# Optimization experiments

Hardware: AMD Instinct MI355X
Metric: run time of the kernel (lower is better)

The kernel has to match this reference:

```python
import jax, jax.numpy as jnp
import numpy as np

IN_C, OUT_C, K = 256, 256, 3

def setup_inputs() -> dict:
    key = jax.random.key(0)
    kx, kw, kb = jax.random.split(key, 3)
    x = jax.random.normal(kx, (32, IN_C, 56, 56), dtype=jnp.float32)
    # kaiming-like scale for conv weight
    fan_in = IN_C * K * K
    weight = jax.random.normal(kw, (OUT_C, IN_C, K, K), dtype=jnp.float32) / np.sqrt(fan_in)
    bias = jax.random.normal(kb, (OUT_C,), dtype=jnp.float32) * 0.01
    return {"x": x, "weight": weight, "bias": bias}

def reference(x, weight, bias):
    # SparseConv2d computes an (approximately lossless, threshold=1e-6)
    # block-sparse conv2d; exact math == dense conv2d, stride 1, pad 1.
    y = jax.lax.conv_general_dilated(
        x, weight,
        window_strides=(1, 1),
        padding=((1, 1), (1, 1)),
        dimension_numbers=("NCHW", "OIHW", "NCHW"),
    )
    return y + bias[None, :, None, None]
```

## Files before the change

### kernel.cpp

```cpp
#include <hip/hip_runtime.h>
#include <hip/hip_bf16.h>

#define IN_C  256
#define OUT_C 256
#define HH 56
#define WW 56
#define NN 32
#define XT_H 58
#define XT_W 64
#define WT_BYTES (8*9*256*32*2)

#define XS_BYTES 24576
#define WS_TAP   8192
#define LDS_TOTAL (2*XS_BYTES + 4*WS_TAP)

using short8 = __attribute__((ext_vector_type(8))) short;
using f32x4  = __attribute__((ext_vector_type(4))) float;

__device__ __forceinline__ void gload_lds16(const void* g, void* l) {
  __builtin_amdgcn_global_load_lds((const __attribute__((address_space(1))) void*)g,
                                   (__attribute__((address_space(3))) void*)l,
                                   16, 0, 0);
}

#define VMWAIT(N) asm volatile("s_waitcnt vmcnt(" #N ")" ::: "memory")

__global__ void k_wconv(const float* __restrict__ w, __hip_bfloat16* __restrict__ wt) {
  int idx = blockIdx.x * 256 + threadIdx.x;
  if (idx >= OUT_C * IN_C * 9) return;
  int kw = idx % 3; int t1 = idx / 3;
  int kh = t1 % 3;  int t2 = t1 / 3;
  int ic = t2 % IN_C; int oc = t2 / IN_C;
  int tap = kh * 3 + kw;
  int chunk = ic >> 5, ic5 = ic & 31;
  wt[(((chunk * 9 + tap) * 256 + oc) * 32) + ic5] = __float2bfloat16(w[idx]);
}

__global__ void k_xpad(__hip_bfloat16* __restrict__ xt) {
  int cell = blockIdx.x * 256 + threadIdx.x;
  if (cell >= NN * XT_H * XT_W) return;
  int wp = cell & 63; int t = cell >> 6;
  int hp = t % XT_H;
  if (hp == 0 || hp == 57 || wp == 0 || wp >= 57) {
    int4 z; z.x = 0; z.y = 0; z.z = 0; z.w = 0;
    int4* p = (int4*)(xt + (size_t)cell * 256);
#pragma unroll
    for (int i = 0; i < 32; ++i) p[i] = z;
  }
}

__global__ void k_xconv(const float* __restrict__ x, __hip_bfloat16* __restrict__ xt) {
  __shared__ __hip_bfloat16 tile[64][58];
  int bid = blockIdx.x;
  int icb = bid & 3; int t = bid >> 2;
  int h = t % HH; int n = t / HH;
  for (int e = threadIdx.x; e < 64 * 56; e += 256) {
    int i = e / 56, w = e - i * 56;
    tile[i][w] = __float2bfloat16(x[(((size_t)n * IN_C + icb * 64 + i) * HH + h) * WW + w]);
  }
  __syncthreads();
  for (int e = threadIdx.x; e < 56 * 64; e += 256) {
    int w = e >> 6, i = e & 63;
    xt[((size_t)(n * XT_H + h + 1) * XT_W + (w + 1)) * 256 + icb * 64 + i] = tile[i][w];
  }
}

__global__ __launch_bounds__(256, 2) void k_conv(
    const __hip_bfloat16* __restrict__ wt, const __hip_bfloat16* __restrict__ xt,
    const float* __restrict__ bias, float* __restrict__ out) {
  extern __shared__ __align__(16) char lds[];
  char* xs_c = lds;
  char* ws_c = lds + 2 * XS_BYTES;

  const int tid  = threadIdx.x;
  const int wid  = tid >> 6, lane = tid & 63;
  const int cc   = lane & 15, g = lane >> 4;
  const int wn   = wid & 1,  wm = wid >> 1;

  const int work = (blockIdx.x & 7) * 112 + (blockIdx.x >> 3);
  const int n  = work / 28;
  const int rem = work - n * 28;
  const int q  = rem >> 1, oh = rem & 1;
  const int h0 = q * 4;

  int xoff[7], rp_[7], wp_[7];
#pragma unroll
  for (int pt = 0; pt < 7; ++pt) {
    int p = wm * 112 + pt * 16 + cc;
    int rp = p / 56, wp = p - rp * 56;
    rp_[pt] = rp; wp_[pt] = wp;
    xoff[pt] = rp * 4096 + wp * 64 + g * 16;
  }
  const int woffb = (wn * 64 + cc) * 64 + g * 16;

  f32x4 acc[4][7];
#pragma unroll
  for (int a = 0; a < 4; ++a)
#pragma unroll
    for (int b = 0; b < 7; ++b) acc[a][b] = (f32x4){0.f, 0.f, 0.f, 0.f};

  const __hip_bfloat16* xtn = xt + (size_t)(n * XT_H + h0) * XT_W * 256;

  auto stage_w = [&](int slot, int tapblk) {
#pragma unroll
    for (int i = 0; i < 2; ++i) {
      int s = wid * 2 + i;
      const __hip_bfloat16* src = wt + (size_t)tapblk * 8192
                                     + (size_t)(oh * 128 + s * 16 + (lane >> 2)) * 32
                                     + (lane & 3) * 8;
      gload_lds16(src, ws_c + slot * WS_TAP + s * 1024);
    }
  };
  auto stage_x = [&](int buf, int ch) {
#pragma unroll
    for (int i = 0; i < 6; ++i) {
      int s = wid * 6 + i;
      int row = s >> 2, colq = s & 3;
      const __hip_bfloat16* src = xtn + (size_t)(row * 64 + colq * 16 + (lane >> 2)) * 256
                                      + ch * 32 + (lane & 3) * 8;
      gload_lds16(src, xs_c + buf * XS_BYTES + row * 4096 + colq * 1024);
    }
  };

  stage_x(0, 0);
  stage_w(0, 0);
  stage_w(1, 1);
  stage_w(2, 2);

#define PHASE(ch_, tap_, NW_, DOW_, DOX_) do {                                        \
    VMWAIT(NW_);                                                                      \
    __builtin_amdgcn_s_barrier();                                                     \
    if (DOW_) stage_w(((ch_) + (tap_) + 3) & 3, (ch_) * 9 + (tap_) + 3);              \
    if (DOX_) stage_x(((ch_) + 1) & 1, (ch_) + 1);                                    \
    const char* wbase = ws_c + (((ch_) + (tap_)) & 3) * WS_TAP;                       \
    const char* xbase = xs_c + ((ch_) & 1) * XS_BYTES;                                \
    short8 xf[7], wf[4];                                                              \
    _Pragma("unroll")                                                                 \
    for (int pt = 0; pt < 7; ++pt)                                                    \
      xf[pt] = *(const short8*)(xbase + xoff[pt] + ((tap_) / 3) * 4096 + ((tap_) % 3) * 64); \
    _Pragma("unroll")                                                                 \
    for (int oct = 0; oct < 4; ++oct)                                                 \
      wf[oct] = *(const short8*)(wbase + woffb + oct * 1024);                         \
    __builtin_amdgcn_s_setprio(1);                                                    \
    _Pragma("unroll")                                                                 \
    for (int oct = 0; oct < 4; ++oct)                                                 \
      _Pragma("unroll")                                                               \
      for (int pt = 0; pt < 7; ++pt)                                                  \
        acc[oct][pt] = __builtin_amdgcn_mfma_f32_16x16x32_bf16(wf[oct], xf[pt], acc[oct][pt], 0, 0, 0); \
    __builtin_amdgcn_s_setprio(0);                                                    \
  } while (0)

  for (int ch = 0; ch < 7; ++ch) {
    PHASE(ch, 0, 4, 1, 1);
    PHASE(ch, 1, 10, 1, 0);
    PHASE(ch, 2, 10, 1, 0);
    PHASE(ch, 3, 10, 1, 0);
    PHASE(ch, 4, 4, 1, 0);
    PHASE(ch, 5, 4, 1, 0);
    PHASE(ch, 6, 4, 1, 0);
    PHASE(ch, 7, 4, 1, 0);
    PHASE(ch, 8, 4, 1, 0);
  }
  PHASE(7, 0, 4, 1, 0);
  PHASE(7, 1, 4, 1, 0);
  PHASE(7, 2, 4, 1, 0);
  PHASE(7, 3, 4, 1, 0);
  PHASE(7, 4, 4, 1, 0);
  PHASE(7, 5, 4, 1, 0);
  PHASE(7, 6, 4, 0, 0);
  PHASE(7, 7, 2, 0, 0);
  PHASE(7, 8, 0, 0, 0);
#undef PHASE

#pragma unroll
  for (int oct = 0; oct < 4; ++oct) {
    const int oc0 = oh * 128 + wn * 64 + oct * 16 + 4 * g;
#pragma unroll
    for (int r = 0; r < 4; ++r) {
      const float bv = bias[oc0 + r];
      const size_t obase = ((size_t)n * OUT_C + (oc0 + r)) * (HH * WW);
#pragma unroll
      for (int pt = 0; pt < 7; ++pt)
        out[obase + (size_t)(h0 + rp_[pt]) * 56 + wp_[pt]] = acc[oct][pt][r] + bv;
    }
  }
}

extern "C" void kernel_launch(void* const* d_in, const int* in_sizes, int n_in,
                              void* d_out, int out_size, void* d_ws, size_t ws_size,
                              hipStream_t stream) {
  const float* x    = (const float*)d_in[0];
  const float* w    = (const float*)d_in[1];
  const float* bias = (const float*)d_in[2];
  float* out        = (float*)d_out;

  __hip_bfloat16* wt = (__hip_bfloat16*)d_ws;
  __hip_bfloat16* xt = (__hip_bfloat16*)((char*)d_ws + WT_BYTES);

  hipFuncSetAttribute((const void*)k_conv,
                      hipFuncAttributeMaxDynamicSharedMemorySize, LDS_TOTAL);

  k_wconv<<<(OUT_C * IN_C * 9 + 255) / 256, 256, 0, stream>>>(w, wt);
  k_xpad <<<(NN * XT_H * XT_W + 255) / 256, 256, 0, stream>>>(xt);
  k_xconv<<<NN * HH * 4, 256, 0, stream>>>(x, xt);
  k_conv <<<NN * 14 * 2, 256, LDS_TOTAL, stream>>>(wt, xt, bias, out);
}
```

Baseline: 154.2 us.

## Fuse prep kernels and load conv weights directly into registers

The three preprocessing kernels (weight transpose, padding, input transpose to bf16) become one prep kernel with vectorised float4 reads and a full-channel LDS transpose per row, which removes two launches and redundant padding writes. In the conv kernel, weights are no longer staged through LDS. Each lane loads its MFMA operand fragments from global memory into registers, double-buffered one tap ahead, and a barrier now runs only once per input-channel chunk instead of every tap. This cuts LDS use and synchronisation, but puts uncached-looking global loads on the critical path of each tap, where latency may not be fully hidden.

```diff
diff --git a/kernel.cpp b/kernel.cpp
--- a/kernel.cpp
+++ b/kernel.cpp
@@ -11,8 +11,7 @@
 #define WT_BYTES (8*9*256*32*2)
 
 #define XS_BYTES 24576
-#define WS_TAP   8192
-#define LDS_TOTAL (2*XS_BYTES + 4*WS_TAP)
+#define LDS_TOTAL (2*XS_BYTES)
 
 using short8 = __attribute__((ext_vector_type(8))) short;
 using f32x4  = __attribute__((ext_vector_type(4))) float;
@@ -25,43 +24,62 @@
 
 #define VMWAIT(N) asm volatile("s_waitcnt vmcnt(" #N ")" ::: "memory")
 
-__global__ void k_wconv(const float* __restrict__ w, __hip_bfloat16* __restrict__ wt) {
-  int idx = blockIdx.x * 256 + threadIdx.x;
-  if (idx >= OUT_C * IN_C * 9) return;
-  int kw = idx % 3; int t1 = idx / 3;
-  int kh = t1 % 3;  int t2 = t1 / 3;
-  int ic = t2 % IN_C; int oc = t2 / IN_C;
-  int tap = kh * 3 + kw;
-  int chunk = ic >> 5, ic5 = ic & 31;
-  wt[(((chunk * 9 + tap) * 256 + oc) * 32) + ic5] = __float2bfloat16(w[idx]);
-}
-
-__global__ void k_xpad(__hip_bfloat16* __restrict__ xt) {
-  int cell = blockIdx.x * 256 + threadIdx.x;
-  if (cell >= NN * XT_H * XT_W) return;
-  int wp = cell & 63; int t = cell >> 6;
-  int hp = t % XT_H;
-  if (hp == 0 || hp == 57 || wp == 0 || wp >= 57) {
-    int4 z; z.x = 0; z.y = 0; z.z = 0; z.w = 0;
-    int4* p = (int4*)(xt + (size_t)cell * 256);
-#pragma unroll
-    for (int i = 0; i < 32; ++i) p[i] = z;
-  }
-}
-
-__global__ void k_xconv(const float* __restrict__ x, __hip_bfloat16* __restrict__ xt) {
-  __shared__ __hip_bfloat16 tile[64][58];
-  int bid = blockIdx.x;
-  int icb = bid & 3; int t = bid >> 2;
-  int h = t % HH; int n = t / HH;
-  for (int e = threadIdx.x; e < 64 * 56; e += 256) {
-    int i = e / 56, w = e - i * 56;
-    tile[i][w] = __float2bfloat16(x[(((size_t)n * IN_C + icb * 64 + i) * HH + h) * WW + w]);
+__global__ void k_prep(const float* __restrict__ x, const float* __restrict__ w,
+                       __hip_bfloat16* __restrict__ wt, __hip_bfloat16* __restrict__ xt) {
+  const int b = blockIdx.x, tid = threadIdx.x;
+
+  if (b >= NN * XT_H) {
+    const int base = (b - NN * XT_H) * 1024;
+#pragma unroll
+    for (int k = 0; k < 4; ++k) {
+      int idx = base + k * 256 + tid;
+      int kw = idx % 3; int t1 = idx / 3;
+      int kh = t1 % 3;  int t2 = t1 / 3;
+      int ic = t2 % IN_C; int oc = t2 / IN_C;
+      int tap = kh * 3 + kw;
+      wt[((((ic >> 5) * 9 + tap) * 256 + oc) * 32) + (ic & 31)] = __float2bfloat16(w[idx]);
+    }
+    return;
+  }
+
+  const int n = b / XT_H, hp = b % XT_H;
+  __hip_bfloat16* row = xt + (size_t)(n * XT_H + hp) * XT_W * 256;
+
+  if (hp == 0 || hp == XT_H - 1) {
+    int4 z; z.x = z.y = z.z = z.w = 0;
+#pragma unroll
+    for (int k = 0; k < 8; ++k) ((int4*)row)[k * 256 + tid] = z;
+    return;
+  }
+
+  const int h = hp - 1;
+  __shared__ __hip_bfloat16 tile[56][264];
+
+  {
+    const int ic = tid;
+    const float* src = x + (((size_t)n * IN_C + ic) * HH + h) * WW;
+#pragma unroll
+    for (int j = 0; j < 14; ++j) {
+      float4 v = ((const float4*)src)[j];
+      tile[4 * j + 0][ic] = __float2bfloat16(v.x);
+      tile[4 * j + 1][ic] = __float2bfloat16(v.y);
+      tile[4 * j + 2][ic] = __float2bfloat16(v.z);
+      tile[4 * j + 3][ic] = __float2bfloat16(v.w);
+    }
+  }
+  {
+    int4 z; z.x = z.y = z.z = z.w = 0;
+    int cell = tid >> 5, s = tid & 31;
+    int wp = (cell == 0) ? 0 : (56 + cell);
+    ((int4*)(row + (size_t)wp * 256))[s] = z;
   }
   __syncthreads();
-  for (int e = threadIdx.x; e < 56 * 64; e += 256) {
-    int w = e >> 6, i = e & 63;
-    xt[((size_t)(n * XT_H + h + 1) * XT_W + (w + 1)) * 256 + icb * 64 + i] = tile[i][w];
+#pragma unroll
+  for (int k = 0; k < 7; ++k) {
+    int e = k * 256 + tid;
+    int wq = e >> 5, seg = e & 31;
+    short8 v = *(const short8*)&tile[wq][seg * 8];
+    *(short8*)(row + (size_t)(wq + 1) * 256 + seg * 8) = v;
   }
 }
 
@@ -70,7 +88,6 @@
     const float* __restrict__ bias, float* __restrict__ out) {
   extern __shared__ __align__(16) char lds[];
   char* xs_c = lds;
-  char* ws_c = lds + 2 * XS_BYTES;
 
   const int tid  = threadIdx.x;
   const int wid  = tid >> 6, lane = tid & 63;
@@ -83,98 +100,89 @@
   const int q  = rem >> 1, oh = rem & 1;
   const int h0 = q * 4;
 
-  int xoff[7], rp_[7], wp_[7];
+  int xoff[7];
 #pragma unroll
   for (int pt = 0; pt < 7; ++pt) {
     int p = wm * 112 + pt * 16 + cc;
     int rp = p / 56, wp = p - rp * 56;
-    rp_[pt] = rp; wp_[pt] = wp;
     xoff[pt] = rp * 4096 + wp * 64 + g * 16;
   }
-  const int woffb = (wn * 64 + cc) * 64 + g * 16;
+  const int ocb = oh * 128 + wn * 64;
+  const __hip_bfloat16* wlane = wt + (size_t)(ocb + cc) * 32 + g * 8;
 
   f32x4 acc[4][7];
 #pragma unroll
   for (int a = 0; a < 4; ++a)
 #pragma unroll
-    for (int b = 0; b < 7; ++b) acc[a][b] = (f32x4){0.f, 0.f, 0.f, 0.f};
+    for (int bb = 0; bb < 7; ++bb) acc[a][bb] = (f32x4){0.f, 0.f, 0.f, 0.f};
 
   const __hip_bfloat16* xtn = xt + (size_t)(n * XT_H + h0) * XT_W * 256;
 
-  auto stage_w = [&](int slot, int tapblk) {
-#pragma unroll
-    for (int i = 0; i < 2; ++i) {
-      int s = wid * 2 + i;
-      const __hip_bfloat16* src = wt + (size_t)tapblk * 8192
-                                     + (size_t)(oh * 128 + s * 16 + (lane >> 2)) * 32
-                                     + (lane & 3) * 8;
-      gload_lds16(src, ws_c + slot * WS_TAP + s * 1024);
-    }
-  };
   auto stage_x = [&](int buf, int ch) {
 #pragma unroll
     for (int i = 0; i < 6; ++i) {
       int s = wid * 6 + i;
-      int row = s >> 2, colq = s & 3;
-      const __hip_bfloat16* src = xtn + (size_t)(row * 64 + colq * 16 + (lane >> 2)) * 256
+      int rowc = s >> 2, colq = s & 3;
+      const __hip_bfloat16* src = xtn + (size_t)(rowc * 64 + colq * 16 + (lane >> 2)) * 256
                                       + ch * 32 + (lane & 3) * 8;
-      gload_lds16(src, xs_c + buf * XS_BYTES + row * 4096 + colq * 1024);
+      gload_lds16(src, xs_c + buf * XS_BYTES + rowc * 4096 + colq * 1024);
     }
   };
+  short8 wfA[4], wfB[4];
+  auto loadw = [&](short8* dst, int ph) {
+#pragma unroll
+    for (int oct = 0; oct < 4; ++oct)
+      dst[oct] = *(const short8*)(wlane + (size_t)ph * 8192 + oct * 512);
+  };
 
   stage_x(0, 0);
-  stage_w(0, 0);
-  stage_w(1, 1);
-  stage_w(2, 2);
-
-#define PHASE(ch_, tap_, NW_, DOW_, DOX_) do {                                        \
-    VMWAIT(NW_);                                                                      \
-    __builtin_amdgcn_s_barrier();                                                     \
-    if (DOW_) stage_w(((ch_) + (tap_) + 3) & 3, (ch_) * 9 + (tap_) + 3);              \
-    if (DOX_) stage_x(((ch_) + 1) & 1, (ch_) + 1);                                    \
-    const char* wbase = ws_c + (((ch_) + (tap_)) & 3) * WS_TAP;                       \
-    const char* xbase = xs_c + ((ch_) & 1) * XS_BYTES;                                \
-    short8 xf[7], wf[4];                                                              \
+  loadw(wfA, 0);
+
+#define PHASE(ch_, tap_, WU_, WL_) do {                                               \
+    if ((tap_) == 0) {                                                                \
+      VMWAIT(4);           \
+      __builtin_amdgcn_s_barrier();                                                   \
+      if ((ch_) < 7) stage_x(((ch_) + 1) & 1, (ch_) + 1);                             \
+    }                                                                                 \
+    if (!((ch_) == 7 && (tap_) == 8)) loadw(WL_, (ch_) * 9 + (tap_) + 1);             \
+    const char* xb = xs_c + (((ch_) & 1) ? XS_BYTES : 0);                             \
+    short8 xf[7];                                                                     \
     _Pragma("unroll")                                                                 \
     for (int pt = 0; pt < 7; ++pt)                                                    \
-      xf[pt] = *(const short8*)(xbase + xoff[pt] + ((tap_) / 3) * 4096 + ((tap_) % 3) * 64); \
-    _Pragma("unroll")                                                                 \
-    for (int oct = 0; oct < 4; ++oct)                                                 \
-      wf[oct] = *(const short8*)(wbase + woffb + oct * 1024);                         \
+      xf[pt] = *(const short8*)(xb + xoff[pt] + ((tap_) / 3) * 4096 + ((tap_) % 3) * 64); \
     __builtin_amdgcn_s_setprio(1);                                                    \
     _Pragma("unroll")                                                                 \
     for (int oct = 0; oct < 4; ++oct)                                                 \
       _Pragma("unroll")                                                               \
       for (int pt = 0; pt < 7; ++pt)                                                  \
-        acc[oct][pt] = __builtin_amdgcn_mfma_f32_16x16x32_bf16(wf[oct], xf[pt], acc[oct][pt], 0, 0, 0); \
+        acc[oct][pt] = __builtin_amdgcn_mfma_f32_16x16x32_bf16(WU_[oct], xf[pt], acc[oct][pt], 0, 0, 0); \
     __builtin_amdgcn_s_setprio(0);                                                    \
   } while (0)
 
-  for (int ch = 0; ch < 7; ++ch) {
-    PHASE(ch, 0, 4, 1, 1);
-    PHASE(ch, 1, 10, 1, 0);
-    PHASE(ch, 2, 10, 1, 0);
-    PHASE(ch, 3, 10, 1, 0);
-    PHASE(ch, 4, 4, 1, 0);
-    PHASE(ch, 5, 4, 1, 0);
-    PHASE(ch, 6, 4, 1, 0);
-    PHASE(ch, 7, 4, 1, 0);
-    PHASE(ch, 8, 4, 1, 0);
-  }
-  PHASE(7, 0, 4, 1, 0);
-  PHASE(7, 1, 4, 1, 0);
-  PHASE(7, 2, 4, 1, 0);
-  PHASE(7, 3, 4, 1, 0);
-  PHASE(7, 4, 4, 1, 0);
-  PHASE(7, 5, 4, 1, 0);
-  PHASE(7, 6, 4, 0, 0);
-  PHASE(7, 7, 2, 0, 0);
-  PHASE(7, 8, 0, 0, 0);
+  for (int ch = 0; ch < 8; ++ch) {
+    PHASE(ch, 0, wfA, wfB);
+    PHASE(ch, 1, wfB, wfA);
+    PHASE(ch, 2, wfA, wfB);
+    PHASE(ch, 3, wfB, wfA);
+    PHASE(ch, 4, wfA, wfB);
+    PHASE(ch, 5, wfB, wfA);
+    PHASE(ch, 6, wfA, wfB);
+    PHASE(ch, 7, wfB, wfA);
+    PHASE(ch, 8, wfA, wfB);
+#pragma unroll
+    for (int oct = 0; oct < 4; ++oct) wfA[oct] = wfB[oct];
+  }
 #undef PHASE
 
+  int rp_[7], wp_[7];
+#pragma unroll
+  for (int pt = 0; pt < 7; ++pt) {
+    int p = wm * 112 + pt * 16 + cc;
+    rp_[pt] = p / 56; wp_[pt] = p - rp_[pt] * 56;
+  }
 #pragma unroll
   for (int oct = 0; oct < 4; ++oct) {
-    const int oc0 = oh * 128 + wn * 64 + oct * 16 + 4 * g;
+    const int oc0 = ocb + oct * 16 + 4 * g;
 #pragma unroll
     for (int r = 0; r < 4; ++r) {
       const float bv = bias[oc0 + r];
@@ -200,8 +208,6 @@
   hipFuncSetAttribute((const void*)k_conv,
                       hipFuncAttributeMaxDynamicSharedMemorySize, LDS_TOTAL);
 
-  k_wconv<<<(OUT_C * IN_C * 9 + 255) / 256, 256, 0, stream>>>(w, wt);
-  k_xpad <<<(NN * XT_H * XT_W + 255) / 256, 256, 0, stream>>>(xt);
-  k_xconv<<<NN * HH * 4, 256, 0, stream>>>(x, xt);
-  k_conv <<<NN * 14 * 2, 256, LDS_TOTAL, stream>>>(wt, xt, bias, out);
-}
+  k_prep<<<NN * XT_H + 576, 256, 0, stream>>>(x, w, wt, xt);
+  k_conv<<<NN * 14 * 2, 256, LDS_TOTAL, stream>>>(wt, xt, bias, out);
+}
```

After: 155.6 us. No clear change (+0.9%).
